# Kernel tuning notes

Measured on AMD Instinct MI355X. Metric: run time of the kernel, lower is better.

## Reference

```python
import jax, jax.numpy as jnp
import numpy as np

N = 50000
E = 600000


def setup_inputs() -> dict:
    key = jax.random.key(0)
    ks = jax.random.split(key, 8)
    x = jax.random.normal(ks[0], (N, 128), dtype=jnp.float32)
    # guarantee every node appears at least once as a source (row) so deg > 0
    row_extra = jax.random.randint(ks[1], (E - N,), 0, N, dtype=jnp.int32)
    row = jnp.concatenate([jnp.arange(N, dtype=jnp.int32), row_extra])
    col = jax.random.randint(ks[2], (E,), 0, N, dtype=jnp.int32)
    edge_index = jnp.stack([row, col])  # [2, E]
    edge_weight = jax.random.uniform(ks[3], (E,), dtype=jnp.float32, minval=0.1, maxval=1.0)
    s1 = 1.0 / np.sqrt(128)
    W1 = jax.random.normal(ks[4], (128, 128), dtype=jnp.float32) * s1
    b1 = jnp.zeros((128,), dtype=jnp.float32)
    W2 = jax.random.normal(ks[5], (128, 128), dtype=jnp.float32) * s1
    b2 = jnp.zeros((128,), dtype=jnp.float32)
    return {"x": x, "edge_index": edge_index, "edge_weight": edge_weight,
            "W1": W1, "b1": b1, "W2": W2, "b2": b2}


def _gcn_layer(x, row, col, edge_weight, W, b):
    # dense linear (torch Linear: x @ W.T + b)
    h = x @ W.T + b  # [N, d_out]
    n = h.shape[0]
    # degree via scatter-add of edge weights over source nodes
    deg = jax.ops.segment_sum(edge_weight, row, num_segments=n)  # [N]
    deg_inv_sqrt = deg ** -0.5
    norm = deg_inv_sqrt[row] * edge_weight * deg_inv_sqrt[col]  # [E]
    # message: gather source features, scale, scatter-add to targets
    msg = norm[:, None] * h[row]  # [E, d_out]
    return jax.ops.segment_sum(msg, col, num_segments=n)  # [N, d_out]


def reference(x, edge_index, edge_weight, W1, b1, W2, b2):
    row, col = edge_index[0], edge_index[1]
    h = _gcn_layer(x, row, col, edge_weight, W1, b1)
    h = jax.nn.relu(h)
    return _gcn_layer(h, row, col, edge_weight, W2, b2)
```

## Files before the change

### kernel.cpp

```cpp
#include <hip/hip_runtime.h>

#define DF 128
#define CAP 40
#define TROWS 64

__global__ __launch_bounds__(256) void build_gemm_kernel(
    const float* __restrict__ X, const float* __restrict__ W,
    const float* __restrict__ b, float* __restrict__ H, int nrows,
    const int* __restrict__ row, const int* __restrict__ col,
    const float* __restrict__ ew,
    float* __restrict__ deg, int* __restrict__ cnt, int2* __restrict__ csr,
    int E, int gemmBlocks)
{
    __shared__ float Xs[TROWS * DF];
    __shared__ float Wsk[32 * DF];

    const int tid = threadIdx.x;

    if (blockIdx.x >= gemmBlocks) {
        int e = (blockIdx.x - gemmBlocks) * 256 + tid;
        if (e < E) {
            int r = row[e], c = col[e];
            float wv = ew[e];
            atomicAdd(&deg[r], wv);
            int pos = atomicAdd(&cnt[c], 1);
            if (pos < CAP)
                csr[(size_t)c * CAP + pos] = make_int2(r, __float_as_int(wv));
        }
        return;
    }

    const int rgrp = tid >> 5;
    const int cgrp = tid & 31;
    const int n0   = blockIdx.x * TROWS;

#pragma unroll
    for (int i = 0; i < 8; ++i) {
        int idx = tid + i * 256;
        int r   = idx >> 5;
        int kk  = idx & 31;
        int n   = n0 + r;
        float4 v = make_float4(0.f, 0.f, 0.f, 0.f);
        if (n < nrows) v = ((const float4*)(X + (size_t)n * DF))[kk];
        ((float4*)Xs)[idx] = v;
    }

    float4 acc[8];
    const float4 bias = ((const float4*)b)[cgrp];
#pragma unroll
    for (int r = 0; r < 8; ++r) acc[r] = bias;

    const float4* Xs4 = (const float4*)Xs;
    const float4* Ws4 = (const float4*)Wsk;

    for (int k0 = 0; k0 < DF; k0 += 32) {
        __syncthreads();
#pragma unroll
        for (int i = 0; i < 4; ++i) {
            int idx = tid + i * 256;
            int c   = idx >> 3;
            int kk  = idx & 7;
            float4 v = ((const float4*)(W + (size_t)c * DF + k0))[kk];
            int kb = kk * 4;
            Wsk[(kb + 0) * DF + c] = v.x;
            Wsk[(kb + 1) * DF + c] = v.y;
            Wsk[(kb + 2) * DF + c] = v.z;
            Wsk[(kb + 3) * DF + c] = v.w;
        }
        __syncthreads();

#pragma unroll
        for (int kk = 0; kk < 8; ++kk) {
            const int kb = (k0 >> 2) + kk;
            float4 w0 = Ws4[(kk * 4 + 0) * 32 + cgrp];
            float4 w1 = Ws4[(kk * 4 + 1) * 32 + cgrp];
            float4 w2 = Ws4[(kk * 4 + 2) * 32 + cgrp];
            float4 w3 = Ws4[(kk * 4 + 3) * 32 + cgrp];
#pragma unroll
            for (int r = 0; r < 8; ++r) {
                float4 x4 = Xs4[(rgrp * 8 + r) * 32 + kb];
                acc[r].x = fmaf(x4.x, w0.x, acc[r].x);
                acc[r].y = fmaf(x4.x, w0.y, acc[r].y);
                acc[r].z = fmaf(x4.x, w0.z, acc[r].z);
                acc[r].w = fmaf(x4.x, w0.w, acc[r].w);
                acc[r].x = fmaf(x4.y, w1.x, acc[r].x);
                acc[r].y = fmaf(x4.y, w1.y, acc[r].y);
                acc[r].z = fmaf(x4.y, w1.z, acc[r].z);
                acc[r].w = fmaf(x4.y, w1.w, acc[r].w);
                acc[r].x = fmaf(x4.z, w2.x, acc[r].x);
                acc[r].y = fmaf(x4.z, w2.y, acc[r].y);
                acc[r].z = fmaf(x4.z, w2.z, acc[r].z);
                acc[r].w = fmaf(x4.z, w2.w, acc[r].w);
                acc[r].x = fmaf(x4.w, w3.x, acc[r].x);
                acc[r].y = fmaf(x4.w, w3.y, acc[r].y);
                acc[r].z = fmaf(x4.w, w3.z, acc[r].z);
                acc[r].w = fmaf(x4.w, w3.w, acc[r].w);
            }
        }
    }

#pragma unroll
    for (int r = 0; r < 8; ++r) {
        int n = n0 + rgrp * 8 + r;
        if (n < nrows) ((float4*)(H + (size_t)n * DF))[cgrp] = acc[r];
    }
}

__global__ __launch_bounds__(64) void normb_kernel(int2* __restrict__ csr,
                                                   const int* __restrict__ cnt,
                                                   const float* __restrict__ deg, int N) {
    const int node = blockIdx.x;
    const int t = threadIdx.x;
    int m = cnt[node];
    if (m > CAP) m = CAP;
    if (t < m) {
        int2 rec = csr[(size_t)node * CAP + t];
        float w = __int_as_float(rec.y);
        w *= rsqrtf(deg[rec.x]) * rsqrtf(deg[node]);
        csr[(size_t)node * CAP + t].y = __float_as_int(w);
    }
}

__global__ __launch_bounds__(256) void gemm_kernel(
    const float* __restrict__ X, const float* __restrict__ W,
    const float* __restrict__ b, float* __restrict__ H, int nrows)
{
    __shared__ float Xs[TROWS * DF];
    __shared__ float Wsk[32 * DF];

    const int tid  = threadIdx.x;
    const int rgrp = tid >> 5;
    const int cgrp = tid & 31;
    const int n0   = blockIdx.x * TROWS;

#pragma unroll
    for (int i = 0; i < 8; ++i) {
        int idx = tid + i * 256;
        int r   = idx >> 5;
        int kk  = idx & 31;
        int n   = n0 + r;
        float4 v = make_float4(0.f, 0.f, 0.f, 0.f);
        if (n < nrows) v = ((const float4*)(X + (size_t)n * DF))[kk];
        ((float4*)Xs)[idx] = v;
    }

    float4 acc[8];
    const float4 bias = ((const float4*)b)[cgrp];
#pragma unroll
    for (int r = 0; r < 8; ++r) acc[r] = bias;

    const float4* Xs4 = (const float4*)Xs;
    const float4* Ws4 = (const float4*)Wsk;

    for (int k0 = 0; k0 < DF; k0 += 32) {
        __syncthreads();
#pragma unroll
        for (int i = 0; i < 4; ++i) {
            int idx = tid + i * 256;
            int c   = idx >> 3;
            int kk  = idx & 7;
            float4 v = ((const float4*)(W + (size_t)c * DF + k0))[kk];
            int kb = kk * 4;
            Wsk[(kb + 0) * DF + c] = v.x;
            Wsk[(kb + 1) * DF + c] = v.y;
            Wsk[(kb + 2) * DF + c] = v.z;
            Wsk[(kb + 3) * DF + c] = v.w;
        }
        __syncthreads();

#pragma unroll
        for (int kk = 0; kk < 8; ++kk) {
            const int kb = (k0 >> 2) + kk;
            float4 w0 = Ws4[(kk * 4 + 0) * 32 + cgrp];
            float4 w1 = Ws4[(kk * 4 + 1) * 32 + cgrp];
            float4 w2 = Ws4[(kk * 4 + 2) * 32 + cgrp];
            float4 w3 = Ws4[(kk * 4 + 3) * 32 + cgrp];
#pragma unroll
            for (int r = 0; r < 8; ++r) {
                float4 x4 = Xs4[(rgrp * 8 + r) * 32 + kb];
                acc[r].x = fmaf(x4.x, w0.x, acc[r].x);
                acc[r].y = fmaf(x4.x, w0.y, acc[r].y);
                acc[r].z = fmaf(x4.x, w0.z, acc[r].z);
                acc[r].w = fmaf(x4.x, w0.w, acc[r].w);
                acc[r].x = fmaf(x4.y, w1.x, acc[r].x);
                acc[r].y = fmaf(x4.y, w1.y, acc[r].y);
                acc[r].z = fmaf(x4.y, w1.z, acc[r].z);
                acc[r].w = fmaf(x4.y, w1.w, acc[r].w);
                acc[r].x = fmaf(x4.z, w2.x, acc[r].x);
                acc[r].y = fmaf(x4.z, w2.y, acc[r].y);
                acc[r].z = fmaf(x4.z, w2.z, acc[r].z);
                acc[r].w = fmaf(x4.z, w2.w, acc[r].w);
                acc[r].x = fmaf(x4.w, w3.x, acc[r].x);
                acc[r].y = fmaf(x4.w, w3.y, acc[r].y);
                acc[r].z = fmaf(x4.w, w3.z, acc[r].z);
                acc[r].w = fmaf(x4.w, w3.w, acc[r].w);
            }
        }
    }

#pragma unroll
    for (int r = 0; r < 8; ++r) {
        int n = n0 + rgrp * 8 + r;
        if (n < nrows) ((float4*)(H + (size_t)n * DF))[cgrp] = acc[r];
    }
}

template <bool RELU_OUT>
__global__ __launch_bounds__(256) void agg_kernel(
    const float4* __restrict__ H4,
    const int2* __restrict__ csr, const int* __restrict__ cnt,
    float4* __restrict__ O4, int N)
{
    const int gid  = blockIdx.x * blockDim.x + threadIdx.x;
    const int node = gid >> 5;
    const int t    = gid & 31;
    if (node >= N) return;
    int m = cnt[node];
    if (m > CAP) m = CAP;
    const int mr = (m + 3) & ~3;
    const int2* bucket = csr + (size_t)node * CAP;

    float4 acc = make_float4(0.f, 0.f, 0.f, 0.f);
    for (int i = 0; i < mr; i += 4) {
        const int2 r0 = bucket[i + 0];
        const int2 r1 = bucket[i + 1];
        const int2 r2 = bucket[i + 2];
        const int2 r3 = bucket[i + 3];
        float4 h0 = H4[(size_t)r0.x * 32 + t];
        float4 h1 = H4[(size_t)r1.x * 32 + t];
        float4 h2 = H4[(size_t)r2.x * 32 + t];
        float4 h3 = H4[(size_t)r3.x * 32 + t];
        const float w0 = __int_as_float(r0.y);
        const float w1 = __int_as_float(r1.y);
        const float w2 = __int_as_float(r2.y);
        const float w3 = __int_as_float(r3.y);
        acc.x = fmaf(w0, h0.x, acc.x); acc.y = fmaf(w0, h0.y, acc.y);
        acc.z = fmaf(w0, h0.z, acc.z); acc.w = fmaf(w0, h0.w, acc.w);
        acc.x = fmaf(w1, h1.x, acc.x); acc.y = fmaf(w1, h1.y, acc.y);
        acc.z = fmaf(w1, h1.z, acc.z); acc.w = fmaf(w1, h1.w, acc.w);
        acc.x = fmaf(w2, h2.x, acc.x); acc.y = fmaf(w2, h2.y, acc.y);
        acc.z = fmaf(w2, h2.z, acc.z); acc.w = fmaf(w2, h2.w, acc.w);
        acc.x = fmaf(w3, h3.x, acc.x); acc.y = fmaf(w3, h3.y, acc.y);
        acc.z = fmaf(w3, h3.z, acc.z); acc.w = fmaf(w3, h3.w, acc.w);
    }
    if (RELU_OUT) {
        acc.x = fmaxf(acc.x, 0.f); acc.y = fmaxf(acc.y, 0.f);
        acc.z = fmaxf(acc.z, 0.f); acc.w = fmaxf(acc.w, 0.f);
    }
    O4[(size_t)node * 32 + t] = acc;
}

extern "C" void kernel_launch(void* const* d_in, const int* in_sizes, int n_in,
                              void* d_out, int out_size, void* d_ws, size_t ws_size,
                              hipStream_t stream) {
    const float* x  = (const float*)d_in[0];
    const int*   ei = (const int*)d_in[1];
    const float* ew = (const float*)d_in[2];
    const float* W1 = (const float*)d_in[3];
    const float* b1 = (const float*)d_in[4];
    const float* W2 = (const float*)d_in[5];
    const float* b2 = (const float*)d_in[6];
    float* out = (float*)d_out;

    const int E = in_sizes[2];
    const int N = in_sizes[0] / DF;
    const int* row = ei;
    const int* col = ei + E;

    char* ws = (char*)d_ws;
    size_t offb = 0;
    auto alloc = [&](size_t bytes) { char* p = ws + offb; offb = (offb + bytes + 511) & ~(size_t)511; return p; };
    float* deg  = (float*)alloc((size_t)2 * N * 4);
    int*   cnt  = (int*)(deg + N);
    int2*  csr  = (int2*)alloc((size_t)N * CAP * 8);
    float* h1   = (float*)alloc((size_t)N * DF * 4);
    float* agg1 = (float*)alloc((size_t)N * DF * 4);
    (void)ws_size;

    hipMemsetAsync(deg, 0, (size_t)2 * N * 4, stream);
    hipMemsetAsync(csr, 0, (size_t)N * CAP * 8, stream);

    const int TB = 256;
    const int eblocks = (E + TB - 1) / TB;
    const int gemm_blocks = (N + TROWS - 1) / TROWS;
    const int agg_blocks = (N * 32 + TB - 1) / TB;

    build_gemm_kernel<<<gemm_blocks + eblocks, 256, 0, stream>>>(
        x, W1, b1, h1, N, row, col, ew, deg, cnt, csr, E, gemm_blocks);

    normb_kernel<<<N, 64, 0, stream>>>(csr, cnt, deg, N);

    agg_kernel<true><<<agg_blocks, TB, 0, stream>>>((const float4*)h1, csr, cnt,
                                                    (float4*)agg1, N);
    gemm_kernel<<<gemm_blocks, 256, 0, stream>>>(agg1, W2, b2, h1, N);
    agg_kernel<false><<<agg_blocks, TB, 0, stream>>>((const float4*)h1, csr, cnt,
                                                     (float4*)out, N);
}
```

Before: 300.1 us.

## Interleave build and GEMM blocks, drop CSR memset, flatten norm kernel, exact agg tail

Edge-scatter blocks are interleaved with GEMM blocks in the fused launch (three build blocks per GEMM block) so the atomic-heavy and compute-heavy work share CUs over time. The normalization kernel is rewritten as a flat 256-thread grid over N*CAP slots instead of one 64-thread block per node. The aggregation loop now handles the remainder exactly with clamped indices and zero weights, which allows the 20MB memset of the CSR buffer to be removed. The risk is that unwritten CSR slots are never read only if the tail logic is correct.

```diff
diff --git a/kernel.cpp b/kernel.cpp
--- a/kernel.cpp
+++ b/kernel.cpp
@@ -10,29 +10,39 @@
     const int* __restrict__ row, const int* __restrict__ col,
     const float* __restrict__ ew,
     float* __restrict__ deg, int* __restrict__ cnt, int2* __restrict__ csr,
-    int E, int gemmBlocks)
+    int E, int gemmBlocks, int buildBlocks)
 {
     __shared__ float Xs[TROWS * DF];
     __shared__ float Wsk[32 * DF];
 
     const int tid = threadIdx.x;
-
-    if (blockIdx.x >= gemmBlocks) {
-        int e = (blockIdx.x - gemmBlocks) * 256 + tid;
-        if (e < E) {
-            int r = row[e], c = col[e];
-            float wv = ew[e];
-            atomicAdd(&deg[r], wv);
-            int pos = atomicAdd(&cnt[c], 1);
-            if (pos < CAP)
-                csr[(size_t)c * CAP + pos] = make_int2(r, __float_as_int(wv));
+    const int r4  = blockIdx.x & 3;
+    const int q   = blockIdx.x >> 2;
+
+    int bidx = -1;
+    if (blockIdx.x >= 4 * gemmBlocks) {
+        bidx = 3 * gemmBlocks + (blockIdx.x - 4 * gemmBlocks);
+    } else if (r4 != 0) {
+        bidx = q * 3 + (r4 - 1);
+    }
+    if (bidx >= 0) {
+        if (bidx < buildBlocks) {
+            int e = bidx * 256 + tid;
+            if (e < E) {
+                int r = row[e], c = col[e];
+                float wv = ew[e];
+                atomicAdd(&deg[r], wv);
+                int pos = atomicAdd(&cnt[c], 1);
+                if (pos < CAP)
+                    csr[(size_t)c * CAP + pos] = make_int2(r, __float_as_int(wv));
+            }
         }
         return;
     }
 
     const int rgrp = tid >> 5;
     const int cgrp = tid & 31;
-    const int n0   = blockIdx.x * TROWS;
+    const int n0   = q * TROWS;
 
 #pragma unroll
     for (int i = 0; i < 8; ++i) {
@@ -106,18 +116,19 @@
     }
 }
 
-__global__ __launch_bounds__(64) void normb_kernel(int2* __restrict__ csr,
-                                                   const int* __restrict__ cnt,
-                                                   const float* __restrict__ deg, int N) {
-    const int node = blockIdx.x;
-    const int t = threadIdx.x;
+__global__ __launch_bounds__(256) void normb_kernel(int2* __restrict__ csr,
+                                                    const int* __restrict__ cnt,
+                                                    const float* __restrict__ deg, int N) {
+    const int gid = blockIdx.x * 256 + threadIdx.x;
+    if (gid >= N * CAP) return;
+    const int node = gid / CAP;
+    const int slot = gid - node * CAP;
     int m = cnt[node];
     if (m > CAP) m = CAP;
-    if (t < m) {
-        int2 rec = csr[(size_t)node * CAP + t];
-        float w = __int_as_float(rec.y);
-        w *= rsqrtf(deg[rec.x]) * rsqrtf(deg[node]);
-        csr[(size_t)node * CAP + t].y = __float_as_int(w);
+    if (slot < m) {
+        int2 rec = csr[gid];
+        float w = __int_as_float(rec.y) * rsqrtf(deg[rec.x]) * rsqrtf(deg[node]);
+        csr[gid].y = __float_as_int(w);
     }
 }
 
@@ -217,11 +228,11 @@
     if (node >= N) return;
     int m = cnt[node];
     if (m > CAP) m = CAP;
-    const int mr = (m + 3) & ~3;
     const int2* bucket = csr + (size_t)node * CAP;
 
     float4 acc = make_float4(0.f, 0.f, 0.f, 0.f);
-    for (int i = 0; i < mr; i += 4) {
+    int i = 0;
+    for (; i + 4 <= m; i += 4) {
         const int2 r0 = bucket[i + 0];
         const int2 r1 = bucket[i + 1];
         const int2 r2 = bucket[i + 2];
@@ -243,6 +254,31 @@
         acc.x = fmaf(w3, h3.x, acc.x); acc.y = fmaf(w3, h3.y, acc.y);
         acc.z = fmaf(w3, h3.z, acc.z); acc.w = fmaf(w3, h3.w, acc.w);
     }
+    if (i < m) {
+        const int i1 = min(i + 1, m - 1);
+        const int i2 = min(i + 2, m - 1);
+        const int i3 = min(i + 3, m - 1);
+        const int2 r0 = bucket[i];
+        const int2 r1 = bucket[i1];
+        const int2 r2 = bucket[i2];
+        const int2 r3 = bucket[i3];
+        float4 h0 = H4[(size_t)r0.x * 32 + t];
+        float4 h1 = H4[(size_t)r1.x * 32 + t];
+        float4 h2 = H4[(size_t)r2.x * 32 + t];
+        float4 h3 = H4[(size_t)r3.x * 32 + t];
+        const float w0 = __int_as_float(r0.y);
+        const float w1 = (i + 1 < m) ? __int_as_float(r1.y) : 0.f;
+        const float w2 = (i + 2 < m) ? __int_as_float(r2.y) : 0.f;
+        const float w3 = (i + 3 < m) ? __int_as_float(r3.y) : 0.f;
+        acc.x = fmaf(w0, h0.x, acc.x); acc.y = fmaf(w0, h0.y, acc.y);
+        acc.z = fmaf(w0, h0.z, acc.z); acc.w = fmaf(w0, h0.w, acc.w);
+        acc.x = fmaf(w1, h1.x, acc.x); acc.y = fmaf(w1, h1.y, acc.y);
+        acc.z = fmaf(w1, h1.z, acc.z); acc.w = fmaf(w1, h1.w, acc.w);
+        acc.x = fmaf(w2, h2.x, acc.x); acc.y = fmaf(w2, h2.y, acc.y);
+        acc.z = fmaf(w2, h2.z, acc.z); acc.w = fmaf(w2, h2.w, acc.w);
+        acc.x = fmaf(w3, h3.x, acc.x); acc.y = fmaf(w3, h3.y, acc.y);
+        acc.z = fmaf(w3, h3.z, acc.z); acc.w = fmaf(w3, h3.w, acc.w);
+    }
     if (RELU_OUT) {
         acc.x = fmaxf(acc.x, 0.f); acc.y = fmaxf(acc.y, 0.f);
         acc.z = fmaxf(acc.z, 0.f); acc.w = fmaxf(acc.w, 0.f);
@@ -278,17 +314,19 @@
     (void)ws_size;
 
     hipMemsetAsync(deg, 0, (size_t)2 * N * 4, stream);
-    hipMemsetAsync(csr, 0, (size_t)N * CAP * 8, stream);
 
     const int TB = 256;
-    const int eblocks = (E + TB - 1) / TB;
-    const int gemm_blocks = (N + TROWS - 1) / TROWS;
+    const int gemm_blocks  = (N + TROWS - 1) / TROWS;
+    const int build_blocks = (E + TB - 1) / TB;
+    int total_blocks = 4 * gemm_blocks;
+    if (build_blocks > 3 * gemm_blocks)
+        total_blocks += build_blocks - 3 * gemm_blocks;
     const int agg_blocks = (N * 32 + TB - 1) / TB;
 
-    build_gemm_kernel<<<gemm_blocks + eblocks, 256, 0, stream>>>(
-        x, W1, b1, h1, N, row, col, ew, deg, cnt, csr, E, gemm_blocks);
-
-    normb_kernel<<<N, 64, 0, stream>>>(csr, cnt, deg, N);
+    build_gemm_kernel<<<total_blocks, 256, 0, stream>>>(
+        x, W1, b1, h1, N, row, col, ew, deg, cnt, csr, E, gemm_blocks, build_blocks);
+
+    normb_kernel<<<(N * CAP + 255) / 256, 256, 0, stream>>>(csr, cnt, deg, N);
 
     agg_kernel<true><<<agg_blocks, TB, 0, stream>>>((const float4*)h1, csr, cnt,
                                                     (float4*)agg1, N);
```

Result: slower. 335.8 us (+11.9%).
